# Kernel optimization log

Measured on AMD Instinct MI355X. Metric: run time of the kernel, lower is better.

Reference implementation:

```python
import jax, jax.numpy as jnp
import numpy as np
import math

NUM_HEADS = 16

def setup_inputs() -> dict:
    key = jax.random.key(0)
    ks = jax.random.split(key, 5)
    d_model = 1024
    std = math.sqrt(2.0 / (d_model + d_model))
    x = jax.random.normal(ks[0], (2, 2048, d_model), dtype=jnp.float32)
    Wq = jax.random.normal(ks[1], (d_model, d_model), dtype=jnp.float32) * std
    Wk = jax.random.normal(ks[2], (d_model, d_model), dtype=jnp.float32) * std
    Wv = jax.random.normal(ks[3], (d_model, d_model), dtype=jnp.float32) * std
    Wo = jax.random.normal(ks[4], (d_model, d_model), dtype=jnp.float32) * std
    return {"x": x, "Wq": Wq, "Wk": Wk, "Wv": Wv, "Wo": Wo}

def reference(x, Wq, Wk, Wv, Wo):
    # x: [b, s, d]; W*: [d_out, d_in]
    b, s, d = x.shape
    h = NUM_HEADS
    dh = d // h
    def proj(W):
        y = jnp.einsum('bsd,ed->bse', x, W)           # [b, s, d]
        return y.reshape(b, s, h, dh).transpose(0, 2, 1, 3)  # [b, h, s, dh]
    Q, K, V = proj(Wq), proj(Wk), proj(Wv)
    scale = 1.0 / math.sqrt(dh)
    logits = jnp.einsum('bhqd,bhkd->bhqk', Q, K) * scale  # [b, h, s, s]
    causal = jnp.tril(jnp.ones((s, s), dtype=bool))
    logits = jnp.where(causal, logits, -jnp.inf)
    attn = jax.nn.softmax(logits, axis=-1)
    out = jnp.einsum('bhqk,bhkd->bhqd', attn, V)          # [b, h, s, dh]
    out = out.transpose(0, 2, 1, 3).reshape(b, s, d)
    return jnp.einsum('bsv,dv->bsd', out, Wo)
```

## Files before the change

kernel.cpp:

```cpp
#include <hip/hip_runtime.h>
#include <hip/hip_bf16.h>
#include <math.h>

typedef unsigned short ushort_t;
typedef __attribute__((ext_vector_type(8))) short bf16x8;
typedef __attribute__((ext_vector_type(4))) float f32x4;

#define MFMA16(a,b,c) __builtin_amdgcn_mfma_f32_16x16x32_bf16(a,b,c,0,0,0)
#define QSCALE 0.1803368801111204f

typedef unsigned int u32;
typedef __attribute__((address_space(1))) const u32* gp1_t;
typedef __attribute__((address_space(3))) u32* lp3_t;

__device__ __forceinline__ void async_copy16(void* l, const void* g) {
    __builtin_amdgcn_global_load_lds((gp1_t)g, (lp3_t)l, 16, 0, 0);
}

__device__ __forceinline__ ushort_t f2bf(float f) {
    unsigned u = __float_as_uint(f);
    unsigned r = u + 0x7fffu + ((u >> 16) & 1u);
    return (ushort_t)(r >> 16);
}

__global__ __launch_bounds__(256) void cvt_kernel(
    const float* __restrict__ x,  const float* __restrict__ wq,
    const float* __restrict__ wk, const float* __restrict__ wv,
    const float* __restrict__ wo, ushort_t* __restrict__ dst)
{
    size_t base = ((size_t)blockIdx.x * 256 + threadIdx.x) * 8;
    const float* src; size_t off;
    if      (base < 4194304ul) { src = x;  off = base; }
    else if (base < 5242880ul) { src = wq; off = base - 4194304ul; }
    else if (base < 6291456ul) { src = wk; off = base - 5242880ul; }
    else if (base < 7340032ul) { src = wv; off = base - 6291456ul; }
    else                       { src = wo; off = base - 7340032ul; }
    float4 a = *(const float4*)(src + off);
    float4 b = *(const float4*)(src + off + 4);
    struct alignas(16) U8 { ushort_t v[8]; } o;
    o.v[0]=f2bf(a.x); o.v[1]=f2bf(a.y); o.v[2]=f2bf(a.z); o.v[3]=f2bf(a.w);
    o.v[4]=f2bf(b.x); o.v[5]=f2bf(b.y); o.v[6]=f2bf(b.z); o.v[7]=f2bf(b.w);
    *(U8*)(dst + base) = o;
}

__global__ __launch_bounds__(512) void gemm_bt(
    const ushort_t* __restrict__ A, const ushort_t* __restrict__ B,
    ushort_t* __restrict__ Oq, ushort_t* __restrict__ Ok,
    ushort_t* __restrict__ Ovt, float* __restrict__ Of, int is_out)
{
    __shared__ ushort_t As[2][128 * 64];
    __shared__ ushort_t Bs[2][128 * 64];
    const int t = threadIdx.x, l = t & 63, w = t >> 6;
    const int l4 = l >> 4, lm = l & 15;
    const int wr = w >> 1, wc = w & 1;

    const int nwg = gridDim.x * gridDim.y;
    const int orig = (int)blockIdx.y * gridDim.x + (int)blockIdx.x;
    const int qq = nwg >> 3;
    const int swz = (orig & 7) * qq + (orig >> 3);
    const int n0 = (swz % gridDim.x) * 128;
    const int m0 = (swz / gridDim.x) * 128;

    const int srow = t >> 3, scol = t & 7;

    f32x4 acc[2][4] = {};

    #pragma unroll
    for (int i = 0; i < 2; ++i) {
        const int row = i * 64 + srow;
        const int c = scol ^ (row & 7);
        async_copy16((char*)&As[0][0] + i * 8192 + t * 16,
                     A + (size_t)(m0 + row) * 1024 + c * 8);
        async_copy16((char*)&Bs[0][0] + i * 8192 + t * 16,
                     B + (size_t)(n0 + row) * 1024 + c * 8);
    }

    for (int kt = 0; kt < 16; ++kt) {
        const int cur = kt & 1;
        if (kt + 1 < 16) {
            const int k0 = (kt + 1) * 64;
            #pragma unroll
            for (int i = 0; i < 2; ++i) {
                const int row = i * 64 + srow;
                const int c = scol ^ (row & 7);
                async_copy16((char*)&As[cur ^ 1][0] + i * 8192 + t * 16,
                             A + (size_t)(m0 + row) * 1024 + k0 + c * 8);
                async_copy16((char*)&Bs[cur ^ 1][0] + i * 8192 + t * 16,
                             B + (size_t)(n0 + row) * 1024 + k0 + c * 8);
            }
            asm volatile("s_waitcnt vmcnt(4)" ::: "memory");
        } else {
            asm volatile("s_waitcnt vmcnt(0)" ::: "memory");
        }
        __builtin_amdgcn_s_barrier();

        #pragma unroll
        for (int ks = 0; ks < 2; ++ks) {
            bf16x8 af[2], bfr[4];
            #pragma unroll
            for (int mi = 0; mi < 2; ++mi) {
                const int row = wr * 32 + mi * 16 + lm;
                const int ch = l4 + 4 * ks;
                af[mi] = *(const bf16x8*)(&As[cur][0] + row * 64 + ((ch ^ (row & 7)) << 3));
            }
            #pragma unroll
            for (int ni = 0; ni < 4; ++ni) {
                const int row = wc * 64 + ni * 16 + lm;
                const int ch = l4 + 4 * ks;
                bfr[ni] = *(const bf16x8*)(&Bs[cur][0] + row * 64 + ((ch ^ (row & 7)) << 3));
            }
            #pragma unroll
            for (int mi = 0; mi < 2; ++mi)
                #pragma unroll
                for (int ni = 0; ni < 4; ++ni)
                    acc[mi][ni] = MFMA16(af[mi], bfr[ni], acc[mi][ni]);
        }
        asm volatile("s_waitcnt lgkmcnt(0)" ::: "memory");
        __builtin_amdgcn_s_barrier();
    }

    const int mb = m0 + wr * 32, nb = n0 + wc * 64;
    if (is_out) {
        #pragma unroll
        for (int mi = 0; mi < 2; ++mi)
            #pragma unroll
            for (int ni = 0; ni < 4; ++ni) {
                const int n = nb + ni * 16 + lm;
                const int mr = mb + mi * 16 + l4 * 4;
                #pragma unroll
                for (int r = 0; r < 4; ++r)
                    Of[(size_t)(mr + r) * 1024 + n] = acc[mi][ni][r];
            }
    } else if (nb >= 2048) {
        #pragma unroll
        for (int mi = 0; mi < 2; ++mi)
            #pragma unroll
            for (int ni = 0; ni < 4; ++ni) {
                const int nv = nb - 2048 + ni * 16 + lm;
                const int m = mb + mi * 16 + l4 * 4;
                const int b = m >> 11, s = m & 2047, h = nv >> 6, d = nv & 63;
                ushort4 pk;
                pk.x = f2bf(acc[mi][ni][0]); pk.y = f2bf(acc[mi][ni][1]);
                pk.z = f2bf(acc[mi][ni][2]); pk.w = f2bf(acc[mi][ni][3]);
                *(ushort4*)(Ovt + (((size_t)(b * 16 + h) * 64 + d) * 2048 + s)) = pk;
            }
    } else {
        ushort_t* O = (nb < 1024) ? Oq : Ok;
        const float qs = (nb < 1024) ? (float)QSCALE : 1.0f;
        const int nbase = nb & 1023;
        #pragma unroll
        for (int mi = 0; mi < 2; ++mi)
            #pragma unroll
            for (int ni = 0; ni < 4; ++ni) {
                const int n = nbase + ni * 16 + lm;
                const int h = n >> 6, d = n & 63;
                #pragma unroll
                for (int r = 0; r < 4; ++r) {
                    const int m = mb + mi * 16 + l4 * 4 + r;
                    const int b = m >> 11, s = m & 2047;
                    O[((size_t)(b * 16 + h) * 2048 + s) * 64 + d] =
                        f2bf(acc[mi][ni][r] * qs);
                }
            }
    }
}

template<bool MASK>
__device__ __forceinline__ void attn_tile(
    const ushort_t* Kbuf, const ushort_t* Vbuf, ushort_t* Pw,
    const bf16x8 (&qf)[2], const bf16x8 ones,
    f32x4 (&o)[4], f32x4& ol, float& m_run,
    int kv0, int qrow, int l4, int lm)
{
    f32x4 sf[4] = {};
    #pragma unroll
    for (int ks = 0; ks < 2; ++ks)
        #pragma unroll
        for (int cf = 0; cf < 4; ++cf) {
            const int rowK = cf * 16 + lm;
            const int ch = l4 + 4 * ks;
            bf16x8 kf = *(const bf16x8*)(Kbuf + rowK * 64 + ((ch ^ (rowK & 7)) << 3));
            sf[cf] = MFMA16(kf, qf[ks], sf[cf]);
        }

    float tmax = -1e30f;
    #pragma unroll
    for (int cf = 0; cf < 4; ++cf)
        #pragma unroll
        for (int r = 0; r < 4; ++r) {
            float v = sf[cf][r];
            if (MASK && (kv0 + cf * 16 + l4 * 4 + r > qrow)) v = -30000.f;
            sf[cf][r] = v;
            tmax = fmaxf(tmax, v);
        }
    tmax = fmaxf(tmax, __shfl_xor(tmax, 16));
    tmax = fmaxf(tmax, __shfl_xor(tmax, 32));

    if (!__all(tmax <= m_run + 8.f)) {
        const float mn = fmaxf(m_run, tmax);
        const float alpha = __builtin_amdgcn_exp2f(m_run - mn);
        #pragma unroll
        for (int df = 0; df < 4; ++df)
            #pragma unroll
            for (int r = 0; r < 4; ++r)
                o[df][r] *= alpha;
        #pragma unroll
        for (int r = 0; r < 4; ++r) ol[r] *= alpha;
        m_run = mn;
    }

    #pragma unroll
    for (int cf = 0; cf < 4; ++cf) {
        float p0 = __builtin_amdgcn_exp2f(sf[cf][0] - m_run);
        float p1 = __builtin_amdgcn_exp2f(sf[cf][1] - m_run);
        float p2 = __builtin_amdgcn_exp2f(sf[cf][2] - m_run);
        float p3 = __builtin_amdgcn_exp2f(sf[cf][3] - m_run);
        __hip_bfloat162 b01 = __float22bfloat162_rn(make_float2(p0, p1));
        __hip_bfloat162 b23 = __float22bfloat162_rn(make_float2(p2, p3));
        uint2 pkv;
        __builtin_memcpy(&pkv.x, &b01, 4);
        __builtin_memcpy(&pkv.y, &b23, 4);
        *(uint2*)&Pw[lm * 72 + cf * 16 + l4 * 4] = pkv;
    }

    #pragma unroll
    for (int ks = 0; ks < 2; ++ks) {
        bf16x8 pf = *(const bf16x8*)&Pw[lm * 72 + ks * 32 + l4 * 8];
        #pragma unroll
        for (int df = 0; df < 4; ++df) {
            const int rowV = df * 16 + lm;
            const int ch = l4 + 4 * ks;
            bf16x8 vf = *(const bf16x8*)(Vbuf + rowV * 64 + ((ch ^ (rowV & 7)) << 3));
            o[df] = MFMA16(vf, pf, o[df]);
        }
        ol = MFMA16(ones, pf, ol);
    }
}

__global__ __launch_bounds__(512) void attn_kernel(
    const ushort_t* __restrict__ Qg, const ushort_t* __restrict__ Kg,
    const ushort_t* __restrict__ Vtg, ushort_t* __restrict__ Og)
{
    __shared__ ushort_t Ks[2][64 * 64];
    __shared__ ushort_t Vs[2][64 * 64];
    __shared__ ushort_t Ps[8][16 * 72];
    const int t = threadIdx.x, l = t & 63, w = t >> 6;
    const int l4 = l >> 4, lm = l & 15;
    const int bh = blockIdx.x;
    const int qt = 15 - (int)blockIdx.y;
    const int q0 = qt * 128, q0w = q0 + w * 16;
    const int qrow = q0w + lm;

    bf16x8 qf[2];
    {
        const ushort_t* qp = Qg + ((size_t)bh * 2048 + qrow) * 64 + l4 * 8;
        qf[0] = *(const bf16x8*)qp;
        qf[1] = *(const bf16x8*)(qp + 32);
    }
    bf16x8 ones;
    #pragma unroll
    for (int i = 0; i < 8; ++i) ones[i] = (short)0x3F80;

    f32x4 o[4] = {};
    f32x4 ol = {};
    float m_run = -1e30f;

    const int nkv = 2 * qt + 2;
    const int srow = t >> 3, scol = t & 7;
    const ushort_t* kg0 = Kg + ((size_t)bh * 2048 + srow) * 64 + (scol ^ (srow & 7)) * 8;
    const ushort_t* vg0 = Vtg + ((size_t)bh * 64 + srow) * 2048 + (scol ^ (srow & 7)) * 8;

    async_copy16((char*)&Ks[0][0] + t * 16, kg0);
    async_copy16((char*)&Vs[0][0] + t * 16, vg0);
    __syncthreads();

    int kt = 0;
    for (; kt < nkv - 2; ++kt) {
        const int cur = kt & 1;
        async_copy16((char*)&Ks[cur ^ 1][0] + t * 16, kg0 + (size_t)(kt + 1) * 4096);
        async_copy16((char*)&Vs[cur ^ 1][0] + t * 16, vg0 + (size_t)(kt + 1) * 64);

        attn_tile<false>(&Ks[cur][0], &Vs[cur][0], &Ps[w][0],
                         qf, ones, o, ol, m_run, kt * 64, qrow, l4, lm);
        __syncthreads();
    }
    for (; kt < nkv; ++kt) {
        const int cur = kt & 1;
        if (kt + 1 < nkv) {
            async_copy16((char*)&Ks[cur ^ 1][0] + t * 16, kg0 + (size_t)(kt + 1) * 4096);
            async_copy16((char*)&Vs[cur ^ 1][0] + t * 16, vg0 + (size_t)(kt + 1) * 64);
        }
        attn_tile<true>(&Ks[cur][0], &Vs[cur][0], &Ps[w][0],
                        qf, ones, o, ol, m_run, kt * 64, qrow, l4, lm);
        __syncthreads();
    }

    const int b = bh >> 4, h = bh & 15;
    const float inv = 1.f / ol[0];
    #pragma unroll
    for (int df = 0; df < 4; ++df) {
        ushort4 pk4;
        pk4.x = f2bf(o[df][0] * inv); pk4.y = f2bf(o[df][1] * inv);
        pk4.z = f2bf(o[df][2] * inv); pk4.w = f2bf(o[df][3] * inv);
        *(ushort4*)&Og[((size_t)(b * 2048 + qrow)) * 1024 + h * 64 + df * 16 + l4 * 4] = pk4;
    }
}

extern "C" void kernel_launch(void* const* d_in, const int* in_sizes, int n_in,
                              void* d_out, int out_size, void* d_ws, size_t ws_size,
                              hipStream_t stream)
{
    const float* x  = (const float*)d_in[0];
    const float* Wq = (const float*)d_in[1];
    const float* Wk = (const float*)d_in[2];
    const float* Wv = (const float*)d_in[3];
    const float* Wo = (const float*)d_in[4];

    ushort_t* ws  = (ushort_t*)d_ws;
    ushort_t* xb  = ws;
    ushort_t* wqb = ws + 4194304;
    ushort_t* wob = ws + 7340032;
    ushort_t* Qw  = ws + 8388608;
    ushort_t* Kw  = ws + 12582912;
    ushort_t* Vtw = ws + 16777216;
    ushort_t* Aow = ws + 20971520;

    cvt_kernel<<<4096, 256, 0, stream>>>(x, Wq, Wk, Wv, Wo, ws);
    gemm_bt<<<dim3(24, 32), 512, 0, stream>>>(xb, wqb, Qw, Kw, Vtw, nullptr, 0);
    attn_kernel<<<dim3(32, 16), 512, 0, stream>>>(Qw, Kw, Vtw, Aow);
    gemm_bt<<<dim3(8, 32), 512, 0, stream>>>(Aow, wob, nullptr, nullptr, nullptr,
                                             (float*)d_out, 1);
}
```

Baseline: 107.6 us.

## Read K/V directly from global memory in attention, drop LDS staging

The attention kernel no longer stages K and V tiles through double-buffered shared memory with async copies and block barriers. Each wave now loads its K and V MFMA fragments straight from global memory, relying on the caches to serve reuse across waves. The block shrinks to 4 waves covering 64 query rows, with twice as many blocks. Barriers and LDS usage go away, but every wave issues uncoalesced global loads with more latency and no explicit prefetch, and K/V reuse within a block drops.

```diff
diff --git a/kernel.cpp b/kernel.cpp
--- a/kernel.cpp
+++ b/kernel.cpp
@@ -167,8 +167,8 @@
 
 template<bool MASK>
 __device__ __forceinline__ void attn_tile(
-    const ushort_t* Kbuf, const ushort_t* Vbuf, ushort_t* Pw,
-    const bf16x8 (&qf)[2], const bf16x8 ones,
+    const ushort_t* __restrict__ Kbh, const ushort_t* __restrict__ Vbh,
+    ushort_t* Pw, const bf16x8 (&qf)[2], const bf16x8 ones,
     f32x4 (&o)[4], f32x4& ol, float& m_run,
     int kv0, int qrow, int l4, int lm)
 {
@@ -177,9 +177,8 @@
     for (int ks = 0; ks < 2; ++ks)
         #pragma unroll
         for (int cf = 0; cf < 4; ++cf) {
-            const int rowK = cf * 16 + lm;
-            const int ch = l4 + 4 * ks;
-            bf16x8 kf = *(const bf16x8*)(Kbuf + rowK * 64 + ((ch ^ (rowK & 7)) << 3));
+            const int rowK = kv0 + cf * 16 + lm;
+            bf16x8 kf = *(const bf16x8*)(Kbh + (size_t)rowK * 64 + (l4 + 4 * ks) * 8);
             sf[cf] = MFMA16(kf, qf[ks], sf[cf]);
         }
 
@@ -229,27 +228,27 @@
         #pragma unroll
         for (int df = 0; df < 4; ++df) {
             const int rowV = df * 16 + lm;
-            const int ch = l4 + 4 * ks;
-            bf16x8 vf = *(const bf16x8*)(Vbuf + rowV * 64 + ((ch ^ (rowV & 7)) << 3));
+            bf16x8 vf = *(const bf16x8*)(Vbh + (size_t)rowV * 2048 + kv0 + (l4 + 4 * ks) * 8);
             o[df] = MFMA16(vf, pf, o[df]);
         }
         ol = MFMA16(ones, pf, ol);
     }
 }
 
-__global__ __launch_bounds__(512) void attn_kernel(
+__global__ __launch_bounds__(256) void attn_kernel(
     const ushort_t* __restrict__ Qg, const ushort_t* __restrict__ Kg,
     const ushort_t* __restrict__ Vtg, ushort_t* __restrict__ Og)
 {
-    __shared__ ushort_t Ks[2][64 * 64];
-    __shared__ ushort_t Vs[2][64 * 64];
-    __shared__ ushort_t Ps[8][16 * 72];
+    __shared__ ushort_t Ps[4][16 * 72];
     const int t = threadIdx.x, l = t & 63, w = t >> 6;
     const int l4 = l >> 4, lm = l & 15;
     const int bh = blockIdx.x;
-    const int qt = 15 - (int)blockIdx.y;
-    const int q0 = qt * 128, q0w = q0 + w * 16;
+    const int qt = 31 - (int)blockIdx.y;
+    const int q0 = qt * 64, q0w = q0 + w * 16;
     const int qrow = q0w + lm;
+
+    const ushort_t* Kbh = Kg + (size_t)bh * 2048 * 64;
+    const ushort_t* Vbh = Vtg + (size_t)bh * 64 * 2048;
 
     bf16x8 qf[2];
     {
@@ -265,35 +264,12 @@
     f32x4 ol = {};
     float m_run = -1e30f;
 
-    const int nkv = 2 * qt + 2;
-    const int srow = t >> 3, scol = t & 7;
-    const ushort_t* kg0 = Kg + ((size_t)bh * 2048 + srow) * 64 + (scol ^ (srow & 7)) * 8;
-    const ushort_t* vg0 = Vtg + ((size_t)bh * 64 + srow) * 2048 + (scol ^ (srow & 7)) * 8;
-
-    async_copy16((char*)&Ks[0][0] + t * 16, kg0);
-    async_copy16((char*)&Vs[0][0] + t * 16, vg0);
-    __syncthreads();
-
-    int kt = 0;
-    for (; kt < nkv - 2; ++kt) {
-        const int cur = kt & 1;
-        async_copy16((char*)&Ks[cur ^ 1][0] + t * 16, kg0 + (size_t)(kt + 1) * 4096);
-        async_copy16((char*)&Vs[cur ^ 1][0] + t * 16, vg0 + (size_t)(kt + 1) * 64);
-
-        attn_tile<false>(&Ks[cur][0], &Vs[cur][0], &Ps[w][0],
-                         qf, ones, o, ol, m_run, kt * 64, qrow, l4, lm);
-        __syncthreads();
-    }
-    for (; kt < nkv; ++kt) {
-        const int cur = kt & 1;
-        if (kt + 1 < nkv) {
-            async_copy16((char*)&Ks[cur ^ 1][0] + t * 16, kg0 + (size_t)(kt + 1) * 4096);
-            async_copy16((char*)&Vs[cur ^ 1][0] + t * 16, vg0 + (size_t)(kt + 1) * 64);
-        }
-        attn_tile<true>(&Ks[cur][0], &Vs[cur][0], &Ps[w][0],
-                        qf, ones, o, ol, m_run, kt * 64, qrow, l4, lm);
-        __syncthreads();
-    }
+    const int last = qt;
+    for (int kt = 0; kt < last; ++kt)
+        attn_tile<false>(Kbh, Vbh, &Ps[w][0], qf, ones, o, ol, m_run,
+                         kt * 64, qrow, l4, lm);
+    attn_tile<true>(Kbh, Vbh, &Ps[w][0], qf, ones, o, ol, m_run,
+                    last * 64, qrow, l4, lm);
 
     const int b = bh >> 4, h = bh & 15;
     const float inv = 1.f / ol[0];
@@ -327,7 +303,7 @@
 
     cvt_kernel<<<4096, 256, 0, stream>>>(x, Wq, Wk, Wv, Wo, ws);
     gemm_bt<<<dim3(24, 32), 512, 0, stream>>>(xb, wqb, Qw, Kw, Vtw, nullptr, 0);
-    attn_kernel<<<dim3(32, 16), 512, 0, stream>>>(Qw, Kw, Vtw, Aow);
+    attn_kernel<<<dim3(32, 32), 256, 0, stream>>>(Qw, Kw, Vtw, Aow);
     gemm_bt<<<dim3(8, 32), 512, 0, stream>>>(Aow, wob, nullptr, nullptr, nullptr,
                                              (float*)d_out, 1);
 }
```

Result: slower. 207.4 us (+92.8%).
